# Kernel optimization log

Hardware: AMD Instinct MI355X
Metric: run time of the kernel (lower is better)

Reference implementation:

```python
import jax, jax.numpy as jnp
import numpy as np

E = 2048        # embed_dim
H = 16          # num_heads
HKV = 4         # num_heads_kv (GQA)
D = 128         # head_dim
DCONV = 4       # causal depthwise conv width
ROT_DIM = 128   # rotary_emb_dim (= head_dim, full rotation)
ROT_BASE = 10000.0
QKV_DIM = D * (H + 2 * HKV)  # 3072
B, S = 2, 2048


def setup_inputs() -> dict:
    key = jax.random.key(0)
    ks = jax.random.split(key, 7)
    return {
        "x": jax.random.normal(ks[0], (B, S, E), jnp.float32),
        "W_in": jax.random.normal(ks[1], (E, QKV_DIM), jnp.float32) * 0.02,
        "b_in": jax.random.normal(ks[2], (QKV_DIM,), jnp.float32) * 0.02,
        "conv_w": jax.random.normal(ks[3], (QKV_DIM, DCONV), jnp.float32) * 0.1,
        "conv_b": jax.random.normal(ks[4], (QKV_DIM,), jnp.float32) * 0.02,
        "W_out": jax.random.normal(ks[5], (E, E), jnp.float32) * 0.02,
        "b_out": jax.random.normal(ks[6], (E,), jnp.float32) * 0.02,
    }


def _rotary_cos_sin(seqlen, dtype):
    # flash_attn RotaryEmbedding: inv_freq over even indices
    inv_freq = 1.0 / (ROT_BASE ** (np.arange(0, ROT_DIM, 2, dtype=np.float32) / ROT_DIM))
    t = np.arange(seqlen, dtype=np.float32)
    freqs = np.outer(t, inv_freq)                      # [S, ROT_DIM/2]
    return jnp.asarray(np.cos(freqs), dtype), jnp.asarray(np.sin(freqs), dtype)


def _apply_rotary(xh, cos, sin):
    # non-interleaved: rotate halves of the first ROT_DIM dims. xh: [B,S,h,D]
    x1 = xh[..., : ROT_DIM // 2]
    x2 = xh[..., ROT_DIM // 2 : ROT_DIM]
    c = cos[None, :, None, :]
    s = sin[None, :, None, :]
    rot = jnp.concatenate([x1 * c - x2 * s, x2 * c + x1 * s], axis=-1)
    return jnp.concatenate([rot, xh[..., ROT_DIM:]], axis=-1)


def _forward(x, W_in, b_in, conv_w, conv_b, W_out, b_out):
    b, s, _ = x.shape
    qkv = x @ W_in + b_in                              # [B,S,QKV_DIM]

    # causal depthwise conv1d (kernel DCONV, left-pad DCONV-1, trim right)
    xp = jnp.pad(qkv, ((0, 0), (DCONV - 1, 0), (0, 0)))
    conv = conv_b
    for k in range(DCONV):
        conv = conv + xp[:, k : k + s, :] * conv_w[:, k]
    qkv = conv                                         # [B,S,QKV_DIM]

    q, kv = jnp.split(qkv, [H * D], axis=-1)
    q = q.reshape(b, s, H, D)
    kv = kv.reshape(b, s, 2, HKV, D)
    k, v = kv[:, :, 0], kv[:, :, 1]                    # [B,S,HKV,D]

    cos, sin = _rotary_cos_sin(s, x.dtype)
    q = _apply_rotary(q, cos, sin)
    k = _apply_rotary(k, cos, sin)

    # GQA: repeat kv heads
    rep = H // HKV
    k = jnp.repeat(k, rep, axis=2)                     # [B,S,H,D]
    v = jnp.repeat(v, rep, axis=2)

    scale = 1.0 / np.sqrt(D)
    scores = jnp.einsum("bqhd,bkhd->bhqk", q, k) * scale
    causal = jnp.tril(jnp.ones((s, s), bool))
    scores = jnp.where(causal[None, None], scores, jnp.finfo(scores.dtype).min)
    probs = jax.nn.softmax(scores, axis=-1)
    ctx = jnp.einsum("bhqk,bkhd->bqhd", probs, v)      # [B,S,H,D]

    return ctx.reshape(b, s, H * D) @ W_out + b_out    # [B,S,E]


def reference(x, W_in, b_in, conv_w, conv_b, W_out, b_out):
    return _forward(x, W_in, b_in, conv_w, conv_b, W_out, b_out)
```

## Files before the change

### kernel.cpp

```cpp
#include <hip/hip_runtime.h>
#include <hip/hip_bf16.h>

#define B_    2
#define S_    2048
#define E_    2048
#define H_    16
#define HKV_  4
#define D_    128
#define QKV_  3072

#define LOG2E  1.4426950408889634f
#define SCALE  0.08838834764831845f
#define SL     0.127517431f
#define DEFER_THR 62.7f

typedef __attribute__((ext_vector_type(8))) short short8;
typedef __attribute__((ext_vector_type(4))) float floatx4;

typedef __attribute__((address_space(1))) const unsigned int gu32;
typedef __attribute__((address_space(3))) unsigned int lu32;

__device__ __forceinline__ void load_lds16(const unsigned short* g, unsigned short* l) {
    __builtin_amdgcn_global_load_lds((gu32*)g, (lu32*)l, 16, 0, 0);
}

__device__ __forceinline__ float b2f(unsigned short u) {
    union { unsigned int i; float f; } v; v.i = ((unsigned int)u) << 16; return v.f;
}
__device__ __forceinline__ unsigned short f2b(float f) {
    union { float f; unsigned int i; } v; v.f = f;
    unsigned int r = v.i + 0x7FFFu + ((v.i >> 16) & 1u);
    return (unsigned short)(r >> 16);
}
__device__ __forceinline__ unsigned int fbits(float f) {
    union { float f; unsigned int i; } v; v.f = f; return v.i;
}
__device__ __forceinline__ float bits2f(unsigned int i) {
    union { unsigned int i; float f; } v; v.i = i; return v.f;
}

template<int N> __device__ __forceinline__ void waitcnt_vm() {
    static_assert(N >= 0 && N <= 16, "vmcnt out of range");
    if constexpr (N == 0) asm volatile("s_waitcnt vmcnt(0)" ::: "memory");
    else if constexpr (N == 4) asm volatile("s_waitcnt vmcnt(4)" ::: "memory");
    else if constexpr (N == 6) asm volatile("s_waitcnt vmcnt(6)" ::: "memory");
    else if constexpr (N == 8) asm volatile("s_waitcnt vmcnt(8)" ::: "memory");
    else asm volatile("s_waitcnt vmcnt(2)" ::: "memory");
}

__global__ __launch_bounds__(256) void cvt_f32_bf16(
    const float* __restrict__ src, unsigned short* __restrict__ dst, int n)
{
    int i = (blockIdx.x * 256 + threadIdx.x) * 4;
    if (i + 3 < n) {
        float4 v = *(const float4*)&src[i];
        ushort4 o;
        o.x = f2b(v.x); o.y = f2b(v.y); o.z = f2b(v.z); o.w = f2b(v.w);
        *(ushort4*)&dst[i] = o;
    }
}

__global__ __launch_bounds__(256) void transpose_f32_bf16(
    const float* __restrict__ src, unsigned short* __restrict__ dst,
    int R, int C)
{
    __shared__ unsigned short tile[32][33];
    const int c0 = blockIdx.x * 32, r0 = blockIdx.y * 32;
    const int tx = threadIdx.x, ty = threadIdx.y;
    #pragma unroll
    for (int i = 0; i < 4; i++)
        tile[ty + 8 * i][tx] = f2b(src[(size_t)(r0 + ty + 8 * i) * C + c0 + tx]);
    __syncthreads();
    #pragma unroll
    for (int i = 0; i < 4; i++)
        dst[(size_t)(c0 + ty + 8 * i) * R + r0 + tx] = tile[tx][ty + 8 * i];
}

__global__ __launch_bounds__(256) void transpose_bf16(
    const unsigned short* __restrict__ src, unsigned short* __restrict__ dst,
    int R, int C)
{
    __shared__ unsigned short tile[32][33];
    const size_t boff = (size_t)blockIdx.z * R * C;
    src += boff; dst += boff;
    const int c0 = blockIdx.x * 32, r0 = blockIdx.y * 32;
    const int tx = threadIdx.x, ty = threadIdx.y;
    #pragma unroll
    for (int i = 0; i < 4; i++)
        tile[ty + 8 * i][tx] = src[(size_t)(r0 + ty + 8 * i) * C + c0 + tx];
    __syncthreads();
    #pragma unroll
    for (int i = 0; i < 4; i++)
        dst[(size_t)(c0 + ty + 8 * i) * R + r0 + tx] = tile[tx][ty + 8 * i];
}

template<int WR, int QR, int LX>
__device__ __forceinline__ void stage_unit8(
    const unsigned short* __restrict__ G, unsigned short* ls,
    int uu, int g0, int K, int k0, int wave, int lane)
{
    #pragma unroll
    for (int l = 0; l < LX; ++l) {
        const int c    = wave * LX + l;
        const int rr   = c / (QR / 8);
        const int row0 = rr * WR + uu * QR + (c % (QR / 8)) * 8;
        const int srow = row0 + (lane >> 3);
        const int sg   = (lane & 7) ^ (lane >> 3);
        load_lds16(&G[(size_t)(g0 + srow) * K + k0 + sg * 8], &ls[row0 * 64]);
    }
}

template<int BN, int WM, int WN, int OUTF32>
__global__ __launch_bounds__(512, 2) void gemm8(
    const unsigned short* __restrict__ A, const unsigned short* __restrict__ Bt,
    const float* __restrict__ bias, void* __restrict__ Cv,
    int M, int N, int K)
{
    constexpr int BM   = 256;
    constexpr int WMR  = BM / WM, WNR = BN / WN;
    constexpr int QMR  = WMR / 2, QNR = WNR / 2;
    constexpr int FM   = QMR / 16, FN = QNR / 16;
    constexpr int LA   = BM / 128, LB = BN / 128;
    constexpr int TILE = (BM + BN) * 64;

    __shared__ unsigned short lds[2 * TILE];

    const int tid  = threadIdx.x;
    const int wave = tid >> 6, lane = tid & 63;
    const int ln   = lane & 15, kq = lane >> 4;
    const int wm   = wave / WN, wn = wave % WN;

    const int nwg = gridDim.x;
    const int wg  = (blockIdx.x & 7) * (nwg >> 3) + (blockIdx.x >> 3);
    const int nbn = N / BN;
    const int m0  = (wg / nbn) * BM, n0 = (wg % nbn) * BN;

    floatx4 acc[2 * FM][2 * FN];
    #pragma unroll
    for (int i = 0; i < 2 * FM; ++i)
        #pragma unroll
        for (int j = 0; j < 2 * FN; ++j) {
            acc[i][j][0] = 0.f; acc[i][j][1] = 0.f;
            acc[i][j][2] = 0.f; acc[i][j][3] = 0.f;
        }

    stage_unit8<WMR, QMR, LA>(A,  &lds[0],       0, m0, K, 0, wave, lane);
    stage_unit8<WNR, QNR, LB>(Bt, &lds[BM * 64], 0, n0, K, 0, wave, lane);
    stage_unit8<WNR, QNR, LB>(Bt, &lds[BM * 64], 1, n0, K, 0, wave, lane);
    stage_unit8<WMR, QMR, LA>(A,  &lds[0],       1, m0, K, 0, wave, lane);
    waitcnt_vm<4>();
    __builtin_amdgcn_s_barrier();

    const int NT = K >> 6;
    int cur = 0;

    for (int t = 0; t < NT - 1; ++t) {
        const unsigned short* Asp = &lds[cur * TILE];
        const unsigned short* Bsp = Asp + BM * 64;
        unsigned short* Ssp = &lds[(cur ^ 1) * TILE];
        const int k1 = (t + 1) << 6;
        #pragma unroll
        for (int p = 0; p < 4; ++p) {
            const int qm = p >> 1, qn = p & 1;
            short8 af[2][FM], bg[2][FN];
            #pragma unroll
            for (int ks = 0; ks < 2; ++ks) {
                #pragma unroll
                for (int i = 0; i < FM; ++i)
                    af[ks][i] = *(const short8*)&Asp[(wm * WMR + qm * QMR + i * 16 + ln) * 64
                                                     + (((ks * 4 + kq) ^ (ln & 7)) * 8)];
                #pragma unroll
                for (int j = 0; j < FN; ++j)
                    bg[ks][j] = *(const short8*)&Bsp[(wn * WNR + qn * QNR + j * 16 + ln) * 64
                                                     + (((ks * 4 + kq) ^ (ln & 7)) * 8)];
            }
            if (p == 0)      stage_unit8<WMR, QMR, LA>(A,  Ssp,           0, m0, K, k1, wave, lane);
            else if (p == 1) stage_unit8<WNR, QNR, LB>(Bt, Ssp + BM * 64, 0, n0, K, k1, wave, lane);
            else if (p == 2) stage_unit8<WNR, QNR, LB>(Bt, Ssp + BM * 64, 1, n0, K, k1, wave, lane);
            else             stage_unit8<WMR, QMR, LA>(A,  Ssp,           1, m0, K, k1, wave, lane);
            __builtin_amdgcn_s_barrier();
            __builtin_amdgcn_s_setprio(1);
            #pragma unroll
            for (int ks = 0; ks < 2; ++ks)
                #pragma unroll
                for (int i = 0; i < FM; ++i)
                    #pragma unroll
                    for (int j = 0; j < FN; ++j)
                        acc[qm * FM + i][qn * FN + j] = __builtin_amdgcn_mfma_f32_16x16x32_bf16(
                            af[ks][i], bg[ks][j], acc[qm * FM + i][qn * FN + j], 0, 0, 0);
            __builtin_amdgcn_s_setprio(0);
            if (p == 0)      waitcnt_vm<2 * LA>();
            else if (p == 1) waitcnt_vm<LA + LB>();
            else if (p == 2) waitcnt_vm<LA + 2 * LB>();
            else             waitcnt_vm<LA + LB>();
            __builtin_amdgcn_s_barrier();
        }
        cur ^= 1;
    }

    asm volatile("s_waitcnt vmcnt(0)" ::: "memory");
    __builtin_amdgcn_s_barrier();
    {
        const unsigned short* Asp = &lds[cur * TILE];
        const unsigned short* Bsp = Asp + BM * 64;
        #pragma unroll
        for (int p = 0; p < 4; ++p) {
            const int qm = p >> 1, qn = p & 1;
            short8 af[2][FM], bg[2][FN];
            #pragma unroll
            for (int ks = 0; ks < 2; ++ks) {
                #pragma unroll
                for (int i = 0; i < FM; ++i)
                    af[ks][i] = *(const short8*)&Asp[(wm * WMR + qm * QMR + i * 16 + ln) * 64
                                                     + (((ks * 4 + kq) ^ (ln & 7)) * 8)];
                #pragma unroll
                for (int j = 0; j < FN; ++j)
                    bg[ks][j] = *(const short8*)&Bsp[(wn * WNR + qn * QNR + j * 16 + ln) * 64
                                                     + (((ks * 4 + kq) ^ (ln & 7)) * 8)];
            }
            __builtin_amdgcn_s_setprio(1);
            #pragma unroll
            for (int ks = 0; ks < 2; ++ks)
                #pragma unroll
                for (int i = 0; i < FM; ++i)
                    #pragma unroll
                    for (int j = 0; j < FN; ++j)
                        acc[qm * FM + i][qn * FN + j] = __builtin_amdgcn_mfma_f32_16x16x32_bf16(
                            af[ks][i], bg[ks][j], acc[qm * FM + i][qn * FN + j], 0, 0, 0);
            __builtin_amdgcn_s_setprio(0);
        }
    }

    #pragma unroll
    for (int nj = 0; nj < 2 * FN; ++nj) {
        const int col = n0 + wn * WNR + nj * 16 + ln;
        const float bv = bias[col];
        #pragma unroll
        for (int mi = 0; mi < 2 * FM; ++mi) {
            const int rowb = m0 + wm * WMR + mi * 16 + kq * 4;
            #pragma unroll
            for (int r = 0; r < 4; ++r) {
                const float val = acc[mi][nj][r] + bv;
                if (OUTF32) ((float*)Cv)[(size_t)(rowb + r) * N + col] = val;
                else ((unsigned short*)Cv)[(size_t)(rowb + r) * N + col] = f2b(val);
            }
        }
    }
}

__device__ __forceinline__ float conv_at(
    const unsigned short* __restrict__ qb, const float* __restrict__ cw,
    const float* __restrict__ cb, int s, int c)
{
    float acc = cb[c];
    const float* w = cw + c * 4;
    #pragma unroll
    for (int t = 0; t < 4; t++) {
        int sp = s - 3 + t;
        if (sp >= 0) acc += b2f(qb[(size_t)sp * QKV_ + c]) * w[t];
    }
    return acc;
}

__global__ __launch_bounds__(256) void conv_rot(
    const unsigned short* __restrict__ qkv, const float* __restrict__ cw,
    const float* __restrict__ cb, unsigned short* __restrict__ qo,
    unsigned short* __restrict__ ko, unsigned short* __restrict__ vo)
{
    const int bs = blockIdx.x;
    const int b = bs >> 11, s = bs & 2047;
    const unsigned short* qb = qkv + (size_t)b * S_ * QKV_;

    for (int it = threadIdx.x; it < 1792; it += 256) {
        if (it < 1280) {
            const int isq = it < 1024;
            const int rel = isq ? it : it - 1024;
            const int head = rel >> 6, d = rel & 63;
            const int c1 = (isq ? head * 128 : 2048 + head * 128) + d;
            float x1 = conv_at(qb, cw, cb, s, c1);
            float x2 = conv_at(qb, cw, cb, s, c1 + 64);
            float inv = exp2f((float)d * -0.2076205059304601f);
            float ang = (float)s * inv;
            float sn, cs;
            __sincosf(ang, &sn, &cs);
            float r1 = x1 * cs - x2 * sn;
            float r2 = x2 * cs + x1 * sn;
            unsigned short* dst = isq
                ? qo + ((size_t)(b * H_   + head) * S_ + s) * D_
                : ko + ((size_t)(b * HKV_ + head) * S_ + s) * D_;
            dst[d]      = f2b(r1);
            dst[d + 64] = f2b(r2);
        } else {
            const int idx = it - 1280;
            const int g = idx >> 7, d = idx & 127;
            float vv = conv_at(qb, cw, cb, s, 2560 + idx);
            vo[((size_t)(b * HKV_ + g) * S_ + s) * D_ + d] = f2b(vv);
        }
    }
}

__global__ __launch_bounds__(512, 4) void attn(
    const unsigned short* __restrict__ q, const unsigned short* __restrict__ k,
    const unsigned short* __restrict__ vT, unsigned short* __restrict__ ctx)
{
    __shared__ unsigned short Ks[2][64 * 128];
    __shared__ unsigned short Vs[2][128 * 64];
    __shared__ unsigned short Ps[8][16][64];

    const int h = blockIdx.x, qy = blockIdx.y, b = blockIdx.z, g = h >> 2;
    const int qt = b ? (15 - qy) : qy;
    const int tid = threadIdx.x, wave = tid >> 6, lane = tid & 63;
    const int ln = lane & 15, kq = lane >> 4;

    const unsigned short* qh = q  + (size_t)(b * H_   + h) * S_ * D_;
    const unsigned short* kh = k  + (size_t)(b * HKV_ + g) * S_ * D_;
    const unsigned short* vh = vT + (size_t)(b * HKV_ + g) * D_ * S_;

    const int rK = (lane >> 4);
    const int pK = lane & 15;
    const int rV = (lane >> 3);
    const int pV = lane & 7;

    const int qrow0 = qt * 128 + wave * 16;

    short8 qf[4];
    #pragma unroll
    for (int f = 0; f < 4; f++)
        qf[f] = *(const short8*)&qh[(size_t)(qrow0 + ln) * D_ + f * 32 + kq * 8];

    floatx4 o[8];
    #pragma unroll
    for (int i = 0; i < 8; i++) { o[i][0] = 0.f; o[i][1] = 0.f; o[i][2] = 0.f; o[i][3] = 0.f; }
    float mr = -INFINITY, lr = 0.f;

    const int KT = 2 * qt + 2;

    {
        #pragma unroll
        for (int c = 0; c < 2; c++) {
            const int chunk = wave * 2 + c;
            int r  = chunk * 4 + rK;
            int gc = pK ^ (r & 15);
            load_lds16(&kh[(size_t)r * D_ + gc * 8], &Ks[0][chunk * 512]);
            int rv = chunk * 8 + rV;
            int gv = pV ^ (rv & 7);
            load_lds16(&vh[(size_t)rv * S_ + gv * 8], &Vs[0][chunk * 512]);
        }
    }

    for (int kt = 0; kt < KT; kt++) {
        const int buf = kt & 1;
        if (kt + 1 < KT) {
            #pragma unroll
            for (int c = 0; c < 2; c++) {
                const int chunk = wave * 2 + c;
                int r  = chunk * 4 + rK;
                int gc = pK ^ (r & 15);
                load_lds16(&kh[(size_t)((kt + 1) * 64 + r) * D_ + gc * 8],
                           &Ks[buf ^ 1][chunk * 512]);
                int rv = chunk * 8 + rV;
                int gv = pV ^ (rv & 7);
                load_lds16(&vh[(size_t)rv * S_ + (kt + 1) * 64 + gv * 8],
                           &Vs[buf ^ 1][chunk * 512]);
            }
            waitcnt_vm<4>();
        } else {
            waitcnt_vm<0>();
        }
        __builtin_amdgcn_s_barrier();

        if (kt * 64 <= qrow0 + 15) {
            floatx4 scv[4];
            #pragma unroll
            for (int nb = 0; nb < 4; nb++) { scv[nb][0]=0.f; scv[nb][1]=0.f; scv[nb][2]=0.f; scv[nb][3]=0.f; }
            __builtin_amdgcn_s_setprio(1);
            #pragma unroll
            for (int ks = 0; ks < 4; ks++) {
                #pragma unroll
                for (int nb = 0; nb < 4; nb++) {
                    short8 kf = *(const short8*)&Ks[buf][(nb * 16 + ln) * 128 + (((ks * 4 + kq) ^ ln) * 8)];
                    scv[nb] = __builtin_amdgcn_mfma_f32_16x16x32_bf16(kf, qf[ks], scv[nb], 0, 0, 0);
                }
            }
            __builtin_amdgcn_s_setprio(0);

            if (kt * 64 + 63 > qrow0) {
                const int qi = qrow0 + ln;
                #pragma unroll
                for (int nb = 0; nb < 4; nb++)
                    #pragma unroll
                    for (int r = 0; r < 4; r++)
                        if (kt * 64 + nb * 16 + kq * 4 + r > qi) scv[nb][r] = -INFINITY;
            }

            float mx = -INFINITY;
            #pragma unroll
            for (int nb = 0; nb < 4; nb++) {
                float a0 = fmaxf(scv[nb][0], scv[nb][1]);
                float a1 = fmaxf(scv[nb][2], scv[nb][3]);
                mx = fmaxf(mx, fmaxf(a0, a1));
            }
            mx = fmaxf(mx, __shfl_xor(mx, 16));
            mx = fmaxf(mx, __shfl_xor(mx, 32));

            float mt = mr, al = 1.0f;
            if (!__all(mx - mr <= DEFER_THR)) {
                mt = fmaxf(mr, mx);
                al = exp2f((mr - mt) * SL);
                mr = mt;
                float alr[4];
                #pragma unroll
                for (int r = 0; r < 4; r++) alr[r] = __shfl(al, kq * 4 + r);
                #pragma unroll
                for (int dn = 0; dn < 8; dn++)
                    #pragma unroll
                    for (int r = 0; r < 4; r++) o[dn][r] *= alr[r];
            }

            float rs = 0.f;
            #pragma unroll
            for (int nb = 0; nb < 4; nb++) {
                const int gct = 2 * nb + (kq >> 1);
                const int pbase = ((gct ^ (ln & 7)) << 3) + ((kq & 1) << 2);
                #pragma unroll
                for (int rr = 0; rr < 2; rr++) {
                    unsigned int u0 = fbits(exp2f((scv[nb][2 * rr]     - mt) * SL));
                    unsigned int u1 = fbits(exp2f((scv[nb][2 * rr + 1] - mt) * SL));
                    rs += bits2f(u0 & 0xFFFF0000u) + bits2f(u1 & 0xFFFF0000u);
                    *(unsigned int*)&Ps[wave][ln][pbase + 2 * rr] =
                        (u0 >> 16) | (u1 & 0xFFFF0000u);
                }
            }
            rs += __shfl_xor(rs, 16);
            rs += __shfl_xor(rs, 32);
            lr = lr * al + rs;

            short8 pa0 = *(const short8*)&Ps[wave][ln][(kq ^ (ln & 7)) << 3];
            short8 pa1 = *(const short8*)&Ps[wave][ln][((4 + kq) ^ (ln & 7)) << 3];
            __builtin_amdgcn_s_setprio(1);
            #pragma unroll
            for (int dn = 0; dn < 8; dn++) {
                short8 b0 = *(const short8*)&Vs[buf][(dn * 16 + ln) * 64 + ((kq ^ (ln & 7)) * 8)];
                o[dn] = __builtin_amdgcn_mfma_f32_16x16x32_bf16(pa0, b0, o[dn], 0, 0, 0);
                short8 b1 = *(const short8*)&Vs[buf][(dn * 16 + ln) * 64 + (((4 + kq) ^ (ln & 7)) * 8)];
                o[dn] = __builtin_amdgcn_mfma_f32_16x16x32_bf16(pa1, b1, o[dn], 0, 0, 0);
            }
            __builtin_amdgcn_s_setprio(0);
        }

        __builtin_amdgcn_s_barrier();
    }

    float lrr[4];
    #pragma unroll
    for (int r = 0; r < 4; r++) lrr[r] = 1.0f / __shfl(lr, kq * 4 + r);
    #pragma unroll
    for (int r = 0; r < 4; r++) {
        size_t rowoff = (size_t)(b * S_ + qrow0 + kq * 4 + r) * (H_ * D_) + h * D_;
        #pragma unroll
        for (int dn = 0; dn < 8; dn++)
            ctx[rowoff + dn * 16 + ln] = f2b(o[dn][r] * lrr[r]);
    }
}

extern "C" void kernel_launch(void* const* d_in, const int* in_sizes, int n_in,
                              void* d_out, int out_size, void* d_ws, size_t ws_size,
                              hipStream_t stream)
{
    const float* x     = (const float*)d_in[0];
    const float* W_in  = (const float*)d_in[1];
    const float* b_in  = (const float*)d_in[2];
    const float* cw    = (const float*)d_in[3];
    const float* cb    = (const float*)d_in[4];
    const float* W_out = (const float*)d_in[5];
    const float* b_out = (const float*)d_in[6];
    float* out = (float*)d_out;
    char* ws = (char*)d_ws;

    const size_t MB = 1024 * 1024;
    unsigned short* WtIn  = (unsigned short*)(ws);
    unsigned short* WtOut = (unsigned short*)(ws + 12 * MB);
    unsigned short* x16   = (unsigned short*)(ws + 20 * MB);
    unsigned short* qkv   = (unsigned short*)(ws + 36 * MB);
    unsigned short* qa    = (unsigned short*)(ws + 60 * MB);
    unsigned short* ka    = (unsigned short*)(ws + 76 * MB);
    unsigned short* va    = (unsigned short*)(ws + 80 * MB);
    unsigned short* vTa   = (unsigned short*)(ws + 84 * MB);
    unsigned short* ctx   = (unsigned short*)(ws + 20 * MB);

    dim3 tb(32, 8);
    hipLaunchKernelGGL(cvt_f32_bf16, dim3(8192), dim3(256), 0, stream, x, x16, 8388608);
    hipLaunchKernelGGL(transpose_f32_bf16, dim3(96, 64), tb, 0, stream, W_in,  WtIn,  2048, 3072);
    hipLaunchKernelGGL(transpose_f32_bf16, dim3(64, 64), tb, 0, stream, W_out, WtOut, 2048, 2048);
    hipLaunchKernelGGL((gemm8<256, 2, 4, 0>), dim3(192), dim3(512), 0, stream,
                       x16, WtIn, b_in, (void*)qkv, 4096, 3072, 2048);
    hipLaunchKernelGGL(conv_rot, dim3(4096), dim3(256), 0, stream, qkv, cw, cb, qa, ka, va);
    hipLaunchKernelGGL(transpose_bf16, dim3(4, 64, 8), tb, 0, stream, va, vTa, 2048, 128);
    hipLaunchKernelGGL(attn, dim3(16, 16, 2), dim3(512), 0, stream, qa, ka, vTa, ctx);
    hipLaunchKernelGGL((gemm8<128, 4, 2, 1>), dim3(256), dim3(512), 0, stream,
                       ctx, WtOut, b_out, (void*)out, 4096, 2048, 2048);
}
```

Baseline: 363.0 us.

## Fold softmax scale into Q, unroll GEMM k-loop by two, relax waitcnts

The softmax scale times log2(e) is now applied to Q during the rotary/conv prep, which removes a multiply per score element in attention; the defer threshold is rescaled to match. The GEMM main loop is unrolled by two with fixed LDS buffer addresses through a macro, and one vmcnt wait is dropped while the others get tighter counts. Scaling Q before the bf16 cast slightly changes rounding. The dropped wait depends on the remaining waits being enough to keep the LDS double buffer correct.

After: 359.1 us. Within noise of the previous version (-1.1%).

```diff
diff --git a/kernel.cpp b/kernel.cpp
--- a/kernel.cpp
+++ b/kernel.cpp
@@ -12,7 +12,7 @@
 #define LOG2E  1.4426950408889634f
 #define SCALE  0.08838834764831845f
 #define SL     0.127517431f
-#define DEFER_THR 62.7f
+#define DEFER_THR 8.0f
 
 typedef __attribute__((ext_vector_type(8))) short short8;
 typedef __attribute__((ext_vector_type(4))) float floatx4;
@@ -40,12 +40,16 @@
 }
 
 template<int N> __device__ __forceinline__ void waitcnt_vm() {
-    static_assert(N >= 0 && N <= 16, "vmcnt out of range");
+    static_assert(N >= 0 && N <= 8, "vmcnt out of range");
     if constexpr (N == 0) asm volatile("s_waitcnt vmcnt(0)" ::: "memory");
+    else if constexpr (N == 1) asm volatile("s_waitcnt vmcnt(1)" ::: "memory");
+    else if constexpr (N == 2) asm volatile("s_waitcnt vmcnt(2)" ::: "memory");
+    else if constexpr (N == 3) asm volatile("s_waitcnt vmcnt(3)" ::: "memory");
     else if constexpr (N == 4) asm volatile("s_waitcnt vmcnt(4)" ::: "memory");
+    else if constexpr (N == 5) asm volatile("s_waitcnt vmcnt(5)" ::: "memory");
     else if constexpr (N == 6) asm volatile("s_waitcnt vmcnt(6)" ::: "memory");
-    else if constexpr (N == 8) asm volatile("s_waitcnt vmcnt(8)" ::: "memory");
-    else asm volatile("s_waitcnt vmcnt(2)" ::: "memory");
+    else if constexpr (N == 7) asm volatile("s_waitcnt vmcnt(7)" ::: "memory");
+    else asm volatile("s_waitcnt vmcnt(8)" ::: "memory");
 }
 
 __global__ __launch_bounds__(256) void cvt_f32_bf16(
@@ -110,6 +114,51 @@
     }
 }
 
+#define GEMM8_KTILE(ASP, BSP, SSP, K1, DO_STAGE)                                   \
+  {                                                                                \
+    const unsigned short* Asp_ = (ASP);                                            \
+    const unsigned short* Bsp_ = (BSP);                                            \
+    unsigned short* Ssp_ = (SSP);                                                  \
+    const int k1_ = (K1);                                                          \
+    _Pragma("unroll")                                                              \
+    for (int p = 0; p < 4; ++p) {                                                  \
+      const int qm = p >> 1, qn = p & 1;                                           \
+      short8 af[2][FM], bg[2][FN];                                                 \
+      _Pragma("unroll")                                                            \
+      for (int ks = 0; ks < 2; ++ks) {                                             \
+        _Pragma("unroll")                                                          \
+        for (int i = 0; i < FM; ++i)                                               \
+          af[ks][i] = *(const short8*)&Asp_[(wm * WMR + qm * QMR + i * 16 + ln) * 64 \
+                                            + (((ks * 4 + kq) ^ (ln & 7)) * 8)];  \
+        _Pragma("unroll")                                                          \
+        for (int j = 0; j < FN; ++j)                                               \
+          bg[ks][j] = *(const short8*)&Bsp_[(wn * WNR + qn * QNR + j * 16 + ln) * 64 \
+                                            + (((ks * 4 + kq) ^ (ln & 7)) * 8)];  \
+      }                                                                            \
+      if (DO_STAGE) {                                                              \
+        if (p == 0)      stage_unit8<WMR, QMR, LA>(A,  Ssp_,           0, m0, K, k1_, wave, lane); \
+        else if (p == 1) stage_unit8<WNR, QNR, LB>(Bt, Ssp_ + BM * 64, 0, n0, K, k1_, wave, lane); \
+        else if (p == 2) stage_unit8<WNR, QNR, LB>(Bt, Ssp_ + BM * 64, 1, n0, K, k1_, wave, lane); \
+        else             stage_unit8<WMR, QMR, LA>(A,  Ssp_,           1, m0, K, k1_, wave, lane); \
+      }                                                                            \
+      __builtin_amdgcn_s_barrier();                                                \
+      __builtin_amdgcn_s_setprio(1);                                               \
+      _Pragma("unroll")                                                            \
+      for (int ks = 0; ks < 2; ++ks)                                               \
+        _Pragma("unroll")                                                          \
+        for (int i = 0; i < FM; ++i)                                               \
+          _Pragma("unroll")                                                        \
+          for (int j = 0; j < FN; ++j)                                             \
+            acc[qm * FM + i][qn * FN + j] = __builtin_amdgcn_mfma_f32_16x16x32_bf16( \
+                af[ks][i], bg[ks][j], acc[qm * FM + i][qn * FN + j], 0, 0, 0);     \
+      __builtin_amdgcn_s_setprio(0);                                               \
+      if (p == 0)      waitcnt_vm<2 * LA>();                                       \
+      else if (p == 1) waitcnt_vm<LA + LB>();                                      \
+      else if (p == 3) waitcnt_vm<LA + LB>();                                      \
+      __builtin_amdgcn_s_barrier();                                                \
+    }                                                                              \
+  }
+
 template<int BN, int WM, int WN, int OUTF32>
 __global__ __launch_bounds__(512, 2) void gemm8(
     const unsigned short* __restrict__ A, const unsigned short* __restrict__ Bt,
@@ -148,88 +197,19 @@
     stage_unit8<WNR, QNR, LB>(Bt, &lds[BM * 64], 0, n0, K, 0, wave, lane);
     stage_unit8<WNR, QNR, LB>(Bt, &lds[BM * 64], 1, n0, K, 0, wave, lane);
     stage_unit8<WMR, QMR, LA>(A,  &lds[0],       1, m0, K, 0, wave, lane);
-    waitcnt_vm<4>();
+    waitcnt_vm<LA + LB>();
     __builtin_amdgcn_s_barrier();
 
     const int NT = K >> 6;
-    int cur = 0;
-
-    for (int t = 0; t < NT - 1; ++t) {
-        const unsigned short* Asp = &lds[cur * TILE];
-        const unsigned short* Bsp = Asp + BM * 64;
-        unsigned short* Ssp = &lds[(cur ^ 1) * TILE];
-        const int k1 = (t + 1) << 6;
-        #pragma unroll
-        for (int p = 0; p < 4; ++p) {
-            const int qm = p >> 1, qn = p & 1;
-            short8 af[2][FM], bg[2][FN];
-            #pragma unroll
-            for (int ks = 0; ks < 2; ++ks) {
-                #pragma unroll
-                for (int i = 0; i < FM; ++i)
-                    af[ks][i] = *(const short8*)&Asp[(wm * WMR + qm * QMR + i * 16 + ln) * 64
-                                                     + (((ks * 4 + kq) ^ (ln & 7)) * 8)];
-                #pragma unroll
-                for (int j = 0; j < FN; ++j)
-                    bg[ks][j] = *(const short8*)&Bsp[(wn * WNR + qn * QNR + j * 16 + ln) * 64
-                                                     + (((ks * 4 + kq) ^ (ln & 7)) * 8)];
-            }
-            if (p == 0)      stage_unit8<WMR, QMR, LA>(A,  Ssp,           0, m0, K, k1, wave, lane);
-            else if (p == 1) stage_unit8<WNR, QNR, LB>(Bt, Ssp + BM * 64, 0, n0, K, k1, wave, lane);
-            else if (p == 2) stage_unit8<WNR, QNR, LB>(Bt, Ssp + BM * 64, 1, n0, K, k1, wave, lane);
-            else             stage_unit8<WMR, QMR, LA>(A,  Ssp,           1, m0, K, k1, wave, lane);
-            __builtin_amdgcn_s_barrier();
-            __builtin_amdgcn_s_setprio(1);
-            #pragma unroll
-            for (int ks = 0; ks < 2; ++ks)
-                #pragma unroll
-                for (int i = 0; i < FM; ++i)
-                    #pragma unroll
-                    for (int j = 0; j < FN; ++j)
-                        acc[qm * FM + i][qn * FN + j] = __builtin_amdgcn_mfma_f32_16x16x32_bf16(
-                            af[ks][i], bg[ks][j], acc[qm * FM + i][qn * FN + j], 0, 0, 0);
-            __builtin_amdgcn_s_setprio(0);
-            if (p == 0)      waitcnt_vm<2 * LA>();
-            else if (p == 1) waitcnt_vm<LA + LB>();
-            else if (p == 2) waitcnt_vm<LA + 2 * LB>();
-            else             waitcnt_vm<LA + LB>();
-            __builtin_amdgcn_s_barrier();
-        }
-        cur ^= 1;
-    }
-
+
+    for (int t = 0; t < NT - 2; t += 2) {
+        GEMM8_KTILE(&lds[0],    &lds[BM * 64],        &lds[TILE], (t + 1) << 6, true);
+        GEMM8_KTILE(&lds[TILE], &lds[TILE + BM * 64], &lds[0],    (t + 2) << 6, true);
+    }
+    GEMM8_KTILE(&lds[0], &lds[BM * 64], &lds[TILE], (NT - 1) << 6, true);
     asm volatile("s_waitcnt vmcnt(0)" ::: "memory");
     __builtin_amdgcn_s_barrier();
-    {
-        const unsigned short* Asp = &lds[cur * TILE];
-        const unsigned short* Bsp = Asp + BM * 64;
-        #pragma unroll
-        for (int p = 0; p < 4; ++p) {
-            const int qm = p >> 1, qn = p & 1;
-            short8 af[2][FM], bg[2][FN];
-            #pragma unroll
-            for (int ks = 0; ks < 2; ++ks) {
-                #pragma unroll
-                for (int i = 0; i < FM; ++i)
-                    af[ks][i] = *(const short8*)&Asp[(wm * WMR + qm * QMR + i * 16 + ln) * 64
-                                                     + (((ks * 4 + kq) ^ (ln & 7)) * 8)];
-                #pragma unroll
-                for (int j = 0; j < FN; ++j)
-                    bg[ks][j] = *(const short8*)&Bsp[(wn * WNR + qn * QNR + j * 16 + ln) * 64
-                                                     + (((ks * 4 + kq) ^ (ln & 7)) * 8)];
-            }
-            __builtin_amdgcn_s_setprio(1);
-            #pragma unroll
-            for (int ks = 0; ks < 2; ++ks)
-                #pragma unroll
-                for (int i = 0; i < FM; ++i)
-                    #pragma unroll
-                    for (int j = 0; j < FN; ++j)
-                        acc[qm * FM + i][qn * FN + j] = __builtin_amdgcn_mfma_f32_16x16x32_bf16(
-                            af[ks][i], bg[ks][j], acc[qm * FM + i][qn * FN + j], 0, 0, 0);
-            __builtin_amdgcn_s_setprio(0);
-        }
-    }
+    GEMM8_KTILE(&lds[TILE], &lds[TILE + BM * 64], &lds[0], 0, false);
 
     #pragma unroll
     for (int nj = 0; nj < 2 * FN; ++nj) {
@@ -283,8 +263,9 @@
             float ang = (float)s * inv;
             float sn, cs;
             __sincosf(ang, &sn, &cs);
-            float r1 = x1 * cs - x2 * sn;
-            float r2 = x2 * cs + x1 * sn;
+            const float sc = isq ? SL : 1.0f;
+            float r1 = (x1 * cs - x2 * sn) * sc;
+            float r2 = (x2 * cs + x1 * sn) * sc;
             unsigned short* dst = isq
                 ? qo + ((size_t)(b * H_   + head) * S_ + s) * D_
                 : ko + ((size_t)(b * HKV_ + head) * S_ + s) * D_;
@@ -406,7 +387,7 @@
             float mt = mr, al = 1.0f;
             if (!__all(mx - mr <= DEFER_THR)) {
                 mt = fmaxf(mr, mx);
-                al = exp2f((mr - mt) * SL);
+                al = exp2f(mr - mt);
                 mr = mt;
                 float alr[4];
                 #pragma unroll
@@ -424,8 +405,8 @@
                 const int pbase = ((gct ^ (ln & 7)) << 3) + ((kq & 1) << 2);
                 #pragma unroll
                 for (int rr = 0; rr < 2; rr++) {
-                    unsigned int u0 = fbits(exp2f((scv[nb][2 * rr]     - mt) * SL));
-                    unsigned int u1 = fbits(exp2f((scv[nb][2 * rr + 1] - mt) * SL));
+                    unsigned int u0 = fbits(exp2f(scv[nb][2 * rr]     - mt));
+                    unsigned int u1 = fbits(exp2f(scv[nb][2 * rr + 1] - mt));
                     rs += bits2f(u0 & 0xFFFF0000u) + bits2f(u1 & 0xFFFF0000u);
                     *(unsigned int*)&Ps[wave][ln][pbase + 2 * rr] =
                         (u0 >> 16) | (u1 & 0xFFFF0000u);
```
